# Kernel optimization log

Measured on AMD Instinct MI355X. Metric: run time of the kernel, lower is better.

The kernel has to match this reference:

```python
import jax, jax.numpy as jnp
import numpy as np

D = 128
N_COLS = 64
EPS = 1e-6
# op MLP index per feature token: mult, add, cos, absdiff, sub_ab, sub_ba, div_ab, div_ba
MLP_IDX = np.array([0, 1, 2, 3, 4, 4, 5, 5])


def setup_inputs() -> dict:
    key = jax.random.key(0)
    ks = jax.random.split(key, 16)
    B = 64
    pairs = np.array([(i, j) for i in range(N_COLS) for j in range(i + 1, N_COLS)], dtype=np.int32)
    P = pairs.shape[0]  # 2016
    s = 0.02
    inp = {
        "x": jax.random.normal(ks[0], (B, N_COLS, D), dtype=jnp.float32),
        "presence": jax.random.randint(ks[1], (B, N_COLS), 0, 2, dtype=jnp.int32),
        "idx_i": jnp.asarray(pairs[:, 0]),
        "idx_j": jnp.asarray(pairs[:, 1]),
        # 6 op MLPs (multiply, add, cosine, abs_diff, subtract, divide): d -> d/2 -> d
        "ops_W1": jax.random.normal(ks[2], (6, D, D // 2), dtype=jnp.float32) * s,
        "ops_b1": jnp.zeros((6, D // 2), dtype=jnp.float32),
        "ops_W2": jax.random.normal(ks[3], (6, D // 2, D), dtype=jnp.float32) * s,
        "ops_b2": jnp.zeros((6, D), dtype=jnp.float32),
        # presence MLP: 4 -> d/2 -> d
        "pres_W1": jax.random.normal(ks[4], (4, D // 2), dtype=jnp.float32) * s,
        "pres_b1": jnp.zeros((D // 2,), dtype=jnp.float32),
        "pres_W2": jax.random.normal(ks[5], (D // 2, D), dtype=jnp.float32) * s,
        "pres_b2": jnp.zeros((D,), dtype=jnp.float32),
        # fusion MLP: 9d -> 2d -> d
        "fus_W1": jax.random.normal(ks[6], (9 * D, 2 * D), dtype=jnp.float32) * s,
        "fus_b1": jnp.zeros((2 * D,), dtype=jnp.float32),
        "fus_W2": jax.random.normal(ks[7], (2 * D, D), dtype=jnp.float32) * s,
        "fus_b2": jnp.zeros((D,), dtype=jnp.float32),
    }
    return inp


def reference(x, presence, idx_i, idx_j,
              ops_W1, ops_b1, ops_W2, ops_b2,
              pres_W1, pres_b1, pres_W2, pres_b2,
              fus_W1, fus_b1, fus_W2, fus_b2):
    B = x.shape[0]
    P = idx_i.shape[0]
    A = x[:, idx_i]  # [B, P, D]
    Bv = x[:, idx_j]  # [B, P, D]
    An = A / (jnp.linalg.norm(A, axis=-1, keepdims=True) + EPS)
    Bn = Bv / (jnp.linalg.norm(Bv, axis=-1, keepdims=True) + EPS)
    # 8 elementwise relation features [8, B, P, D]
    feats = jnp.stack([
        A * Bv,                 # multiply
        A + Bv,                 # add
        An * Bn,                # cosine (elementwise normalized product)
        jnp.abs(A - Bv),        # abs diff
        A - Bv,                 # subtract A->B
        Bv - A,                 # subtract B->A
        A / (Bv + EPS),         # divide A/B
        Bv / (A + EPS),         # divide B/A
    ])
    W1 = ops_W1[MLP_IDX]  # [8, D, D/2]
    b1 = ops_b1[MLP_IDX]
    W2 = ops_W2[MLP_IDX]
    b2 = ops_b2[MLP_IDX]
    h = jax.nn.relu(jnp.einsum('kbpd,kdh->kbph', feats, W1) + b1[:, None, None, :])
    tok = jnp.einsum('kbph,khd->kbpd', h, W2) + b2[:, None, None, :]  # [8, B, P, D]
    # presence flags [B, P, 4]
    pa = presence[:, idx_i].astype(x.dtype)
    pb = presence[:, idx_j].astype(x.dtype)
    flags = jnp.stack([pa * pb, pa * (1 - pb), (1 - pa) * pb, (1 - pa) * (1 - pb)], axis=-1)
    ptok = jax.nn.relu(flags @ pres_W1 + pres_b1) @ pres_W2 + pres_b2  # [B, P, D]
    # concat 9 tokens -> fusion MLP -> 1 token per pair
    cat = jnp.concatenate([jnp.transpose(tok, (1, 2, 0, 3)).reshape(B, P, 8 * D), ptok], axis=-1)
    out = jax.nn.relu(cat @ fus_W1 + fus_b1) @ fus_W2 + fus_b2  # [B, P, D]
    return out
```

## Files before the change

### kernel.cpp

```cpp
#include <hip/hip_runtime.h>

#define EPS 1e-6f

using bfrag = __attribute__((ext_vector_type(8))) short;
using ffrag = __attribute__((ext_vector_type(4))) float;
typedef unsigned short ushortT;

#define MFMA(a, b, c) __builtin_amdgcn_mfma_f32_16x16x32_bf16((a), (b), (c), 0, 0, 0)

__device__ __forceinline__ ushortT bf_hi(float x) {
  unsigned u = __builtin_bit_cast(unsigned, x);
  return (ushortT)((u + 0x7FFFu + ((u >> 16) & 1u)) >> 16);
}
__device__ __forceinline__ float uaf(unsigned u) { return __builtin_bit_cast(float, u); }
__device__ __forceinline__ unsigned cvtpk(float a, float b) {
  unsigned d;
  asm("v_cvt_pk_bf16_f32 %0, %1, %2" : "=v"(d) : "v"(a), "v"(b));
  return d;
}
__device__ __forceinline__ int op_of(int k) { return (k < 4) ? k : ((k >> 1) + 2); }

__constant__ const int KMAP_host_dummy = 0;

__global__ void prologue(const float* __restrict__ ops_W1,
                         const float* __restrict__ ops_W2,
                         const float* __restrict__ ops_b2,
                         const float* __restrict__ pres_W1,
                         const float* __restrict__ pres_b1,
                         const float* __restrict__ pres_W2,
                         const float* __restrict__ pres_b2,
                         const float* __restrict__ fus_W1,
                         const float* __restrict__ fus_b1,
                         const float* __restrict__ fus_W2,
                         ushortT* __restrict__ Gp,
                         ushortT* __restrict__ W1p,
                         ushortT* __restrict__ W2p,
                         float* __restrict__ cb) {
  const int blk = blockIdx.x;
  const int tid = threadIdx.x;

  if (blk < 512) {
    int r = blk, n = tid;
    int slot = r >> 6;
    const int KMAP[8] = {0, 2, 3, 4, 1, 5, 6, 7};
    int k = KMAP[slot];
    int op = op_of(k);
    const float* w2 = ops_W2 + (size_t)(op * 64 + (r & 63)) * 128;
    const float* w1 = fus_W1 + (size_t)(k * 128) * 256 + n;
    float a0 = 0.f, a1 = 0.f, a2 = 0.f, a3 = 0.f;
#pragma unroll 8
    for (int d = 0; d < 128; d += 4) {
      a0 = fmaf(w2[d], w1[(size_t)d * 256], a0);
      a1 = fmaf(w2[d + 1], w1[(size_t)(d + 1) * 256], a1);
      a2 = fmaf(w2[d + 2], w1[(size_t)(d + 2) * 256], a2);
      a3 = fmaf(w2[d + 3], w1[(size_t)(d + 3) * 256], a3);
    }
    float acc = (a0 + a1) + (a2 + a3);
    int nt = n >> 4, kk = r >> 5, quad = (r >> 3) & 3, j = r & 7;
    int lane = quad * 16 + (n & 15);
    Gp[((nt * 16 + kk) * 64 + lane) * 8 + j] = bf_hi(acc);
  } else if (blk < 544) {
    int gid = (blk - 512) * 256 + tid;
    int lane = gid & 63, kk = (gid >> 6) & 3, nt = (gid >> 8) & 3, k = gid >> 10;
    int op = op_of(k);
    int col = nt * 16 + (lane & 15);
#pragma unroll
    for (int j = 0; j < 8; ++j) {
      int d = kk * 32 + ((lane >> 4) & 3) * 8 + j;
      W1p[gid * 8 + j] = bf_hi(ops_W1[((size_t)op * 128 + d) * 64 + col]);
    }
  } else if (blk < 560) {
    int gid = (blk - 544) * 256 + tid;
    int lane = gid & 63, kk = (gid >> 6) & 7, nt = gid >> 9;
    int col = nt * 16 + (lane & 15);
#pragma unroll
    for (int j = 0; j < 8; ++j) {
      int d = kk * 32 + ((lane >> 4) & 3) * 8 + j;
      W2p[gid * 8 + j] = bf_hi(fus_W2[(size_t)d * 128 + col]);
    }
  } else {
    int c = blk - 560, n = tid;
    __shared__ float hrelu[64];
    __shared__ float ptok[128];
    if (n < 64) hrelu[n] = fmaxf(pres_W1[c * 64 + n] + pres_b1[n], 0.f);
    __syncthreads();
    if (n < 128) {
      float p0 = pres_b2[n], p1 = 0.f;
#pragma unroll 8
      for (int hh = 0; hh < 64; hh += 2) {
        p0 = fmaf(hrelu[hh], pres_W2[hh * 128 + n], p0);
        p1 = fmaf(hrelu[hh + 1], pres_W2[(hh + 1) * 128 + n], p1);
      }
      ptok[n] = p0 + p1;
    }
    __syncthreads();
    float acc = fus_b1[n];
#pragma unroll 4
    for (int d = 0; d < 128; ++d)
      acc = fmaf(ptok[d], fus_W1[(size_t)(1024 + d) * 256 + n], acc);
    float acc2 = 0.f;
    for (int k = 0; k < 8; ++k) {
      int op = op_of(k);
#pragma unroll 4
      for (int d = 0; d < 128; ++d)
        acc2 = fmaf(ops_b2[op * 128 + d], fus_W1[(size_t)(k * 128 + d) * 256 + n], acc2);
    }
    cb[c * 256 + n] = acc + acc2;
  }
}

__device__ __forceinline__ void ldX(const float* Xrow, int quad, float (&r)[32]) {
#pragma unroll
  for (int kk = 0; kk < 4; ++kk) {
    float4 t0 = *(const float4*)(Xrow + kk * 32 + quad * 8);
    float4 t1 = *(const float4*)(Xrow + kk * 32 + quad * 8 + 4);
    r[kk * 8 + 0] = t0.x; r[kk * 8 + 1] = t0.y; r[kk * 8 + 2] = t0.z; r[kk * 8 + 3] = t0.w;
    r[kk * 8 + 4] = t1.x; r[kk * 8 + 5] = t1.y; r[kk * 8 + 6] = t1.z; r[kk * 8 + 7] = t1.w;
  }
}

struct Frag2 {
  bfrag h[4];
  bfrag l[4];
};

union U4 {
  unsigned u[4];
  bfrag b;
};

#define FM_MUL 0
#define FM_ADD 1
#define FM_SUB 2
#define FM_DAB 3
#define FM_DBA 4

template <int M>
__device__ __forceinline__ void buildFrags(const float (&af)[32], const float (&bf)[32],
                                           Frag2& fr) {
#pragma unroll
  for (int kk = 0; kk < 4; ++kk) {
    U4 uh, ul;
#pragma unroll
    for (int p = 0; p < 4; ++p) {
      float a0 = af[kk * 8 + 2 * p],     b0 = bf[kk * 8 + 2 * p];
      float a1 = af[kk * 8 + 2 * p + 1], b1 = bf[kk * 8 + 2 * p + 1];
      float f0, f1;
      if constexpr (M == FM_MUL)      { f0 = a0 * b0; f1 = a1 * b1; }
      else if constexpr (M == FM_ADD) { f0 = a0 + b0; f1 = a1 + b1; }
      else if constexpr (M == FM_SUB) { f0 = a0 - b0; f1 = a1 - b1; }
      else if constexpr (M == FM_DAB) {
        f0 = a0 * __builtin_amdgcn_rcpf(b0 + EPS);
        f1 = a1 * __builtin_amdgcn_rcpf(b1 + EPS);
      } else {
        f0 = b0 * __builtin_amdgcn_rcpf(a0 + EPS);
        f1 = b1 * __builtin_amdgcn_rcpf(a1 + EPS);
      }
      unsigned dh = cvtpk(f0, f1);
      float r0 = f0 - uaf(dh << 16);
      float r1 = f1 - uaf(dh & 0xFFFF0000u);
      uh.u[p] = dh;
      ul.u[p] = cvtpk(r0, r1);
    }
    fr.h[kk] = uh.b;
    fr.l[kk] = ul.b;
  }
}

template <int K>
__device__ __forceinline__ ffrag mmW1(const Frag2& fr, int wv, int lane,
                                      const ushortT* __restrict__ W1p) {
  const ushortT* wp = W1p + ((K * 4 + wv) * 4) * 512 + lane * 8;
  ffrag s = {0.f, 0.f, 0.f, 0.f};
#pragma unroll
  for (int kk = 0; kk < 4; ++kk) {
    bfrag w = *(const bfrag*)(wp + kk * 512);
    s = MFMA(fr.h[kk], w, s);
    s = MFMA(fr.l[kk], w, s);
  }
  return s;
}

template <int K>
__device__ __forceinline__ ffrag mmW1Abs(const Frag2& fr, int wv, int lane,
                                         const ushortT* __restrict__ W1p) {
  const ushortT* wp = W1p + ((K * 4 + wv) * 4) * 512 + lane * 8;
  ffrag s = {0.f, 0.f, 0.f, 0.f};
#pragma unroll
  for (int kk = 0; kk < 4; ++kk) {
    U4 h, l, ha, la;
    h.b = fr.h[kk];
    l.b = fr.l[kk];
#pragma unroll
    for (int p = 0; p < 4; ++p) {
      ha.u[p] = h.u[p] & 0x7FFF7FFFu;
      la.u[p] = l.u[p] ^ (h.u[p] & 0x80008000u);
    }
    bfrag w = *(const bfrag*)(wp + kk * 512);
    s = MFMA(ha.b, w, s);
    s = MFMA(la.b, w, s);
  }
  return s;
}

__device__ __forceinline__ void storeH(ffrag s, float scl, float bias, int rbase, int col,
                                       ushortT (*Hh)[136], ushortT (*Hl)[136]) {
  float v[4];
#pragma unroll
  for (int i = 0; i < 4; ++i) v[i] = fmaxf(fmaf(s[i], scl, bias), 0.f);
#pragma unroll
  for (int p = 0; p < 2; ++p) {
    unsigned dh = cvtpk(v[2 * p], v[2 * p + 1]);
    float r0 = v[2 * p] - uaf(dh << 16);
    float r1 = v[2 * p + 1] - uaf(dh & 0xFFFF0000u);
    unsigned dl = cvtpk(r0, r1);
    Hh[rbase + 2 * p][col] = (ushortT)(dh & 0xFFFFu);
    Hh[rbase + 2 * p + 1][col] = (ushortT)(dh >> 16);
    Hl[rbase + 2 * p][col] = (ushortT)(dl & 0xFFFFu);
    Hl[rbase + 2 * p + 1][col] = (ushortT)(dl >> 16);
  }
}

__device__ __forceinline__ void p3round(int r, int wv, int lane, int quad, int c0,
                                        ushortT (*Hh)[136], ushortT (*Hl)[136],
                                        const ushortT* __restrict__ Gp,
                                        ffrag (&u)[4], ffrag (&v)[4]) {
#pragma unroll
  for (int kk = 0; kk < 4; ++kk) {
    bfrag ah0 = *(const bfrag*)&Hh[c0][kk * 32 + quad * 8];
    bfrag al0 = *(const bfrag*)&Hl[c0][kk * 32 + quad * 8];
    bfrag ah1 = *(const bfrag*)&Hh[16 + c0][kk * 32 + quad * 8];
    bfrag al1 = *(const bfrag*)&Hl[16 + c0][kk * 32 + quad * 8];
#pragma unroll
    for (int nt4 = 0; nt4 < 4; ++nt4) {
      bfrag g = *(const bfrag*)(Gp + (((wv * 4 + nt4) * 16 + r * 4 + kk) * 64 + lane) * 8);
      u[nt4] = MFMA(ah0, g, u[nt4]);
      u[nt4] = MFMA(al0, g, u[nt4]);
      v[nt4] = MFMA(ah1, g, v[nt4]);
      v[nt4] = MFMA(al1, g, v[nt4]);
    }
  }
}

__global__ __launch_bounds__(256, 3)
void drel_main(const float* __restrict__ x, const int* __restrict__ presence,
               const int* __restrict__ idx_i, const int* __restrict__ idx_j,
               const float* __restrict__ ops_b1, const float* __restrict__ fus_b2,
               const ushortT* __restrict__ W1p, const ushortT* __restrict__ Gp,
               const ushortT* __restrict__ W2p, const float* __restrict__ cbias,
               float* __restrict__ out) {
  __shared__ __align__(16) char smem[51328];
  float   (*Xs)[132]  = reinterpret_cast<float(*)[132]>(smem);
  ushortT (*Hh)[136]  = reinterpret_cast<ushortT(*)[136]>(smem + 33792);
  ushortT (*Hl)[136]  = reinterpret_cast<ushortT(*)[136]>(smem + 42496);
  ushortT (*Dh)[264]  = reinterpret_cast<ushortT(*)[264]>(smem + 33792);
  int* sCombo = reinterpret_cast<int*>(smem + 51200);

  const int tid = threadIdx.x;
  const int wv = tid >> 6, lane = tid & 63, quad = lane >> 4, c0 = lane & 15;

  const int blk = blockIdx.x;
  const int b = blk / 63;
  const int p0 = (blk % 63) * 32;

  const float* xb = x + (size_t)b * 64 * 128;
#pragma unroll
  for (int it = 0; it < 8; ++it) {
    int i = tid + it * 256;
    int row = i >> 5, c4 = (i & 31) * 4;
    *(float4*)&Xs[row][c4] = *(const float4*)(xb + row * 128 + c4);
  }
  if (tid < 32) {
    int p = p0 + tid;
    int pa = presence[b * 64 + idx_i[p]];
    int pb = presence[b * 64 + idx_j[p]];
    sCombo[tid] = pa ? (pb ? 0 : 1) : (pb ? 2 : 3);
  }

  const int ri0 = idx_i[p0 + c0],      rj0 = idx_j[p0 + c0];
  const int ri1 = idx_i[p0 + 16 + c0], rj1 = idx_j[p0 + 16 + c0];

  const int bcol = wv * 16 + c0;
  const float bb0 = ops_b1[0 * 64 + bcol];
  const float bb1_ = ops_b1[1 * 64 + bcol];
  const float bb2 = ops_b1[2 * 64 + bcol];
  const float bb3 = ops_b1[3 * 64 + bcol];
  const float bb4 = ops_b1[4 * 64 + bcol];
  const float bb5 = ops_b1[5 * 64 + bcol];

  ffrag u[4], v[4];
  __syncthreads();
  {
    int comb0[4], comb1[4];
#pragma unroll
    for (int i = 0; i < 4; ++i) {
      comb0[i] = sCombo[quad * 4 + i];
      comb1[i] = sCombo[16 + quad * 4 + i];
    }
#pragma unroll
    for (int nt4 = 0; nt4 < 4; ++nt4) {
      int col = (wv * 4 + nt4) * 16 + c0;
#pragma unroll
      for (int i = 0; i < 4; ++i) {
        u[nt4][i] = cbias[comb0[i] * 256 + col];
        v[nt4][i] = cbias[comb1[i] * 256 + col];
      }
    }
  }

  float af[32], bf[32];
  ffrag s4t0, s4t1;

  {
    ldX(Xs[ri0], quad, af); ldX(Xs[rj0], quad, bf);
    float sa = 0.f, sb = 0.f;
#pragma unroll
    for (int q = 0; q < 32; ++q) { sa = fmaf(af[q], af[q], sa); sb = fmaf(bf[q], bf[q], sb); }
    sa += __shfl_xor(sa, 16); sb += __shfl_xor(sb, 16);
    sa += __shfl_xor(sa, 32); sb += __shfl_xor(sb, 32);
    float scl = (1.f / (sqrtf(sa) + EPS)) * (1.f / (sqrtf(sb) + EPS));
    Frag2 fr;
    buildFrags<FM_MUL>(af, bf, fr);
    ffrag s0 = mmW1<0>(fr, wv, lane, W1p);
    ffrag s2 = mmW1<2>(fr, wv, lane, W1p);
    storeH(s0, 1.f, bb0, 0 * 16 + quad * 4, bcol, Hh, Hl);
    storeH(s2, scl, bb2, 0 * 16 + quad * 4, 64 + bcol, Hh, Hl);

    ldX(Xs[ri1], quad, af); ldX(Xs[rj1], quad, bf);
    sa = 0.f; sb = 0.f;
#pragma unroll
    for (int q = 0; q < 32; ++q) { sa = fmaf(af[q], af[q], sa); sb = fmaf(bf[q], bf[q], sb); }
    sa += __shfl_xor(sa, 16); sb += __shfl_xor(sb, 16);
    sa += __shfl_xor(sa, 32); sb += __shfl_xor(sb, 32);
    scl = (1.f / (sqrtf(sa) + EPS)) * (1.f / (sqrtf(sb) + EPS));
    buildFrags<FM_MUL>(af, bf, fr);
    s0 = mmW1<0>(fr, wv, lane, W1p);
    s2 = mmW1<2>(fr, wv, lane, W1p);
    storeH(s0, 1.f, bb0, 1 * 16 + quad * 4, bcol, Hh, Hl);
    storeH(s2, scl, bb2, 1 * 16 + quad * 4, 64 + bcol, Hh, Hl);
  }
  __syncthreads();
  p3round(0, wv, lane, quad, c0, Hh, Hl, Gp, u, v);
  __syncthreads();

  {
    ldX(Xs[ri0], quad, af); ldX(Xs[rj0], quad, bf);
    Frag2 fr;
    buildFrags<FM_SUB>(af, bf, fr);
    s4t0 = mmW1<4>(fr, wv, lane, W1p);
    ffrag s3 = mmW1Abs<3>(fr, wv, lane, W1p);
    storeH(s3, 1.f, bb3, 0 * 16 + quad * 4, bcol, Hh, Hl);
    storeH(s4t0, 1.f, bb4, 0 * 16 + quad * 4, 64 + bcol, Hh, Hl);

    ldX(Xs[ri1], quad, af); ldX(Xs[rj1], quad, bf);
    buildFrags<FM_SUB>(af, bf, fr);
    s4t1 = mmW1<4>(fr, wv, lane, W1p);
    s3 = mmW1Abs<3>(fr, wv, lane, W1p);
    storeH(s3, 1.f, bb3, 1 * 16 + quad * 4, bcol, Hh, Hl);
    storeH(s4t1, 1.f, bb4, 1 * 16 + quad * 4, 64 + bcol, Hh, Hl);
  }
  __syncthreads();
  p3round(1, wv, lane, quad, c0, Hh, Hl, Gp, u, v);
  __syncthreads();

  {
    ldX(Xs[ri0], quad, af); ldX(Xs[rj0], quad, bf);
    Frag2 fr;
    buildFrags<FM_ADD>(af, bf, fr);
    ffrag s1 = mmW1<1>(fr, wv, lane, W1p);
    storeH(s1, 1.f, bb1_, 0 * 16 + quad * 4, bcol, Hh, Hl);
    storeH(s4t0, -1.f, bb4, 0 * 16 + quad * 4, 64 + bcol, Hh, Hl);

    ldX(Xs[ri1], quad, af); ldX(Xs[rj1], quad, bf);
    buildFrags<FM_ADD>(af, bf, fr);
    s1 = mmW1<1>(fr, wv, lane, W1p);
    storeH(s1, 1.f, bb1_, 1 * 16 + quad * 4, bcol, Hh, Hl);
    storeH(s4t1, -1.f, bb4, 1 * 16 + quad * 4, 64 + bcol, Hh, Hl);
  }
  __syncthreads();
  p3round(2, wv, lane, quad, c0, Hh, Hl, Gp, u, v);
  __syncthreads();

  {
    ldX(Xs[ri0], quad, af); ldX(Xs[rj0], quad, bf);
    Frag2 fr;
    buildFrags<FM_DAB>(af, bf, fr);
    ffrag s6 = mmW1<6>(fr, wv, lane, W1p);
    buildFrags<FM_DBA>(af, bf, fr);
    ffrag s7 = mmW1<7>(fr, wv, lane, W1p);
    storeH(s6, 1.f, bb5, 0 * 16 + quad * 4, bcol, Hh, Hl);
    storeH(s7, 1.f, bb5, 0 * 16 + quad * 4, 64 + bcol, Hh, Hl);

    ldX(Xs[ri1], quad, af); ldX(Xs[rj1], quad, bf);
    buildFrags<FM_DAB>(af, bf, fr);
    s6 = mmW1<6>(fr, wv, lane, W1p);
    buildFrags<FM_DBA>(af, bf, fr);
    s7 = mmW1<7>(fr, wv, lane, W1p);
    storeH(s6, 1.f, bb5, 1 * 16 + quad * 4, bcol, Hh, Hl);
    storeH(s7, 1.f, bb5, 1 * 16 + quad * 4, 64 + bcol, Hh, Hl);
  }
  __syncthreads();
  p3round(3, wv, lane, quad, c0, Hh, Hl, Gp, u, v);
  __syncthreads();

#pragma unroll
  for (int nt4 = 0; nt4 < 4; ++nt4) {
    int col = (wv * 4 + nt4) * 16 + c0;
#pragma unroll
    for (int p = 0; p < 2; ++p) {
      unsigned du = cvtpk(fmaxf(u[nt4][2 * p], 0.f), fmaxf(u[nt4][2 * p + 1], 0.f));
      Dh[quad * 4 + 2 * p][col] = (ushortT)(du & 0xFFFFu);
      Dh[quad * 4 + 2 * p + 1][col] = (ushortT)(du >> 16);
      unsigned dv = cvtpk(fmaxf(v[nt4][2 * p], 0.f), fmaxf(v[nt4][2 * p + 1], 0.f));
      Dh[16 + quad * 4 + 2 * p][col] = (ushortT)(dv & 0xFFFFu);
      Dh[16 + quad * 4 + 2 * p + 1][col] = (ushortT)(dv >> 16);
    }
  }
  __syncthreads();

  ffrag o[2], q[2];
#pragma unroll
  for (int nt2 = 0; nt2 < 2; ++nt2) {
    float bias = fus_b2[(wv * 2 + nt2) * 16 + c0];
    o[nt2] = ffrag{bias, bias, bias, bias};
    q[nt2] = o[nt2];
  }
#pragma unroll
  for (int kk = 0; kk < 8; ++kk) {
    bfrag dh0 = *(const bfrag*)&Dh[c0][kk * 32 + quad * 8];
    bfrag dh1 = *(const bfrag*)&Dh[16 + c0][kk * 32 + quad * 8];
#pragma unroll
    for (int nt2 = 0; nt2 < 2; ++nt2) {
      bfrag w = *(const bfrag*)(W2p + (((wv * 2 + nt2) * 8 + kk) * 64 + lane) * 8);
      o[nt2] = MFMA(dh0, w, o[nt2]);
      q[nt2] = MFMA(dh1, w, q[nt2]);
    }
  }
#pragma unroll
  for (int nt2 = 0; nt2 < 2; ++nt2) {
    int col = (wv * 2 + nt2) * 16 + c0;
#pragma unroll
    for (int i = 0; i < 4; ++i) {
      int row = quad * 4 + i;
      out[(size_t)(b * 2016 + p0 + row) * 128 + col] = o[nt2][i];
      out[(size_t)(b * 2016 + p0 + 16 + row) * 128 + col] = q[nt2][i];
    }
  }
}

extern "C" void kernel_launch(void* const* d_in, const int* in_sizes, int n_in,
                              void* d_out, int out_size, void* d_ws, size_t ws_size,
                              hipStream_t stream) {
  const float* x        = (const float*)d_in[0];
  const int*   presence = (const int*)d_in[1];
  const int*   idx_i    = (const int*)d_in[2];
  const int*   idx_j    = (const int*)d_in[3];
  const float* ops_W1   = (const float*)d_in[4];
  const float* ops_b1   = (const float*)d_in[5];
  const float* ops_W2   = (const float*)d_in[6];
  const float* ops_b2   = (const float*)d_in[7];
  const float* pres_W1  = (const float*)d_in[8];
  const float* pres_b1  = (const float*)d_in[9];
  const float* pres_W2  = (const float*)d_in[10];
  const float* pres_b2  = (const float*)d_in[11];
  const float* fus_W1   = (const float*)d_in[12];
  const float* fus_b1   = (const float*)d_in[13];
  const float* fus_W2   = (const float*)d_in[14];
  const float* fus_b2   = (const float*)d_in[15];

  char* ws = (char*)d_ws;
  ushortT* Gp  = (ushortT*)(ws);
  ushortT* W1p = (ushortT*)(ws + 262144);
  ushortT* W2p = (ushortT*)(ws + 393216);
  float*   CB  = (float*)(ws + 458752);

  prologue<<<564, 256, 0, stream>>>(ops_W1, ops_W2, ops_b2, pres_W1, pres_b1,
                                    pres_W2, pres_b2, fus_W1, fus_b1, fus_W2,
                                    Gp, W1p, W2p, CB);
  drel_main<<<4032, 256, 0, stream>>>(x, presence, idx_i, idx_j, ops_b1, fus_b2,
                                      W1p, Gp, W2p, CB, (float*)d_out);
}
```

Baseline: 281.7 us.

## Split first-layer op MLP work across waves by pair tile and op role

Each wave now owns one 16-pair tile and one op (role) and computes all four 16-column output tiles of that op's hidden layer, instead of every wave doing both pair tiles and both ops for one column slice. This removes redundant feature building, norm computation and frag conversion, since each wave builds fragments only for its own op and tile. The abs-diff op now builds its own fragments with fabsf instead of bit-masking subtract fragments. The cost is that each wave loads all W1 column tiles for its op, and waves with different roles may do unequal work, notably in round 2 where the subtract-reuse role only stores.

After: 259.8 us. 7.8% less time.

```diff
diff --git a/kernel.cpp b/kernel.cpp
--- a/kernel.cpp
+++ b/kernel.cpp
@@ -19,8 +19,6 @@
   return d;
 }
 __device__ __forceinline__ int op_of(int k) { return (k < 4) ? k : ((k >> 1) + 2); }
-
-__constant__ const int KMAP_host_dummy = 0;
 
 __global__ void prologue(const float* __restrict__ ops_W1,
                          const float* __restrict__ ops_W2,
@@ -132,8 +130,9 @@
 #define FM_MUL 0
 #define FM_ADD 1
 #define FM_SUB 2
-#define FM_DAB 3
-#define FM_DBA 4
+#define FM_ABS 3
+#define FM_DAB 4
+#define FM_DBA 5
 
 template <int M>
 __device__ __forceinline__ void buildFrags(const float (&af)[32], const float (&bf)[32],
@@ -149,6 +148,7 @@
       if constexpr (M == FM_MUL)      { f0 = a0 * b0; f1 = a1 * b1; }
       else if constexpr (M == FM_ADD) { f0 = a0 + b0; f1 = a1 + b1; }
       else if constexpr (M == FM_SUB) { f0 = a0 - b0; f1 = a1 - b1; }
+      else if constexpr (M == FM_ABS) { f0 = fabsf(a0 - b0); f1 = fabsf(a1 - b1); }
       else if constexpr (M == FM_DAB) {
         f0 = a0 * __builtin_amdgcn_rcpf(b0 + EPS);
         f1 = a1 * __builtin_amdgcn_rcpf(b1 + EPS);
@@ -168,39 +168,26 @@
 }
 
 template <int K>
-__device__ __forceinline__ ffrag mmW1(const Frag2& fr, int wv, int lane,
-                                      const ushortT* __restrict__ W1p) {
-  const ushortT* wp = W1p + ((K * 4 + wv) * 4) * 512 + lane * 8;
-  ffrag s = {0.f, 0.f, 0.f, 0.f};
-#pragma unroll
-  for (int kk = 0; kk < 4; ++kk) {
-    bfrag w = *(const bfrag*)(wp + kk * 512);
-    s = MFMA(fr.h[kk], w, s);
-    s = MFMA(fr.l[kk], w, s);
-  }
-  return s;
-}
-
-template <int K>
-__device__ __forceinline__ ffrag mmW1Abs(const Frag2& fr, int wv, int lane,
-                                         const ushortT* __restrict__ W1p) {
-  const ushortT* wp = W1p + ((K * 4 + wv) * 4) * 512 + lane * 8;
-  ffrag s = {0.f, 0.f, 0.f, 0.f};
-#pragma unroll
-  for (int kk = 0; kk < 4; ++kk) {
-    U4 h, l, ha, la;
-    h.b = fr.h[kk];
-    l.b = fr.l[kk];
-#pragma unroll
-    for (int p = 0; p < 4; ++p) {
-      ha.u[p] = h.u[p] & 0x7FFF7FFFu;
-      la.u[p] = l.u[p] ^ (h.u[p] & 0x80008000u);
-    }
-    bfrag w = *(const bfrag*)(wp + kk * 512);
-    s = MFMA(ha.b, w, s);
-    s = MFMA(la.b, w, s);
-  }
-  return s;
+__device__ __forceinline__ void mmAll(const Frag2& fr, int lane,
+                                      const ushortT* __restrict__ W1p, ffrag (&s)[4]) {
+#pragma unroll
+  for (int nt = 0; nt < 4; ++nt) {
+    const ushortT* wp = W1p + ((K * 4 + nt) * 4) * 512 + lane * 8;
+    ffrag acc = {0.f, 0.f, 0.f, 0.f};
+#pragma unroll
+    for (int kk = 0; kk < 4; ++kk) {
+      bfrag w = *(const bfrag*)(wp + kk * 512);
+      acc = MFMA(fr.h[kk], w, acc);
+      acc = MFMA(fr.l[kk], w, acc);
+    }
+    s[nt] = acc;
+  }
+}
+
+__device__ __forceinline__ void ldBias(const float* __restrict__ ops_b1, int OP, int c0,
+                                       float (&bb)[4]) {
+#pragma unroll
+  for (int nt = 0; nt < 4; ++nt) bb[nt] = ops_b1[OP * 64 + nt * 16 + c0];
 }
 
 __device__ __forceinline__ void storeH(ffrag s, float scl, float bias, int rbase, int col,
@@ -219,6 +206,14 @@
     Hl[rbase + 2 * p][col] = (ushortT)(dl & 0xFFFFu);
     Hl[rbase + 2 * p + 1][col] = (ushortT)(dl >> 16);
   }
+}
+
+__device__ __forceinline__ void storeH4(const ffrag (&s)[4], float scl, const float (&bb)[4],
+                                        int rbase, int colbase, int c0,
+                                        ushortT (*Hh)[136], ushortT (*Hl)[136]) {
+#pragma unroll
+  for (int nt = 0; nt < 4; ++nt)
+    storeH(s[nt], scl, bb[nt], rbase, colbase + nt * 16 + c0, Hh, Hl);
 }
 
 __device__ __forceinline__ void p3round(int r, int wv, int lane, int quad, int c0,
@@ -258,6 +253,8 @@
 
   const int tid = threadIdx.x;
   const int wv = tid >> 6, lane = tid & 63, quad = lane >> 4, c0 = lane & 15;
+  const int wtile = wv & 1;
+  const int wrole = wv >> 1;
 
   const int blk = blockIdx.x;
   const int b = blk / 63;
@@ -277,16 +274,9 @@
     sCombo[tid] = pa ? (pb ? 0 : 1) : (pb ? 2 : 3);
   }
 
-  const int ri0 = idx_i[p0 + c0],      rj0 = idx_j[p0 + c0];
-  const int ri1 = idx_i[p0 + 16 + c0], rj1 = idx_j[p0 + 16 + c0];
-
-  const int bcol = wv * 16 + c0;
-  const float bb0 = ops_b1[0 * 64 + bcol];
-  const float bb1_ = ops_b1[1 * 64 + bcol];
-  const float bb2 = ops_b1[2 * 64 + bcol];
-  const float bb3 = ops_b1[3 * 64 + bcol];
-  const float bb4 = ops_b1[4 * 64 + bcol];
-  const float bb5 = ops_b1[5 * 64 + bcol];
+  const int rI = idx_i[p0 + wtile * 16 + c0];
+  const int rJ = idx_j[p0 + wtile * 16 + c0];
+  const int rbase = wtile * 16 + quad * 4;
 
   ffrag u[4], v[4];
   __syncthreads();
@@ -309,95 +299,86 @@
   }
 
   float af[32], bf[32];
-  ffrag s4t0, s4t1;
+  Frag2 fr;
+  ffrag s4[4];
 
   {
-    ldX(Xs[ri0], quad, af); ldX(Xs[rj0], quad, bf);
-    float sa = 0.f, sb = 0.f;
-#pragma unroll
-    for (int q = 0; q < 32; ++q) { sa = fmaf(af[q], af[q], sa); sb = fmaf(bf[q], bf[q], sb); }
-    sa += __shfl_xor(sa, 16); sb += __shfl_xor(sb, 16);
-    sa += __shfl_xor(sa, 32); sb += __shfl_xor(sb, 32);
-    float scl = (1.f / (sqrtf(sa) + EPS)) * (1.f / (sqrtf(sb) + EPS));
-    Frag2 fr;
+    ldX(Xs[rI], quad, af); ldX(Xs[rJ], quad, bf);
     buildFrags<FM_MUL>(af, bf, fr);
-    ffrag s0 = mmW1<0>(fr, wv, lane, W1p);
-    ffrag s2 = mmW1<2>(fr, wv, lane, W1p);
-    storeH(s0, 1.f, bb0, 0 * 16 + quad * 4, bcol, Hh, Hl);
-    storeH(s2, scl, bb2, 0 * 16 + quad * 4, 64 + bcol, Hh, Hl);
-
-    ldX(Xs[ri1], quad, af); ldX(Xs[rj1], quad, bf);
-    sa = 0.f; sb = 0.f;
-#pragma unroll
-    for (int q = 0; q < 32; ++q) { sa = fmaf(af[q], af[q], sa); sb = fmaf(bf[q], bf[q], sb); }
-    sa += __shfl_xor(sa, 16); sb += __shfl_xor(sb, 16);
-    sa += __shfl_xor(sa, 32); sb += __shfl_xor(sb, 32);
-    scl = (1.f / (sqrtf(sa) + EPS)) * (1.f / (sqrtf(sb) + EPS));
-    buildFrags<FM_MUL>(af, bf, fr);
-    s0 = mmW1<0>(fr, wv, lane, W1p);
-    s2 = mmW1<2>(fr, wv, lane, W1p);
-    storeH(s0, 1.f, bb0, 1 * 16 + quad * 4, bcol, Hh, Hl);
-    storeH(s2, scl, bb2, 1 * 16 + quad * 4, 64 + bcol, Hh, Hl);
+    ffrag s[4];
+    float bb[4];
+    if (wrole == 0) {
+      ldBias(ops_b1, 0, c0, bb);
+      mmAll<0>(fr, lane, W1p, s);
+      storeH4(s, 1.f, bb, rbase, 0, c0, Hh, Hl);
+    } else {
+      float sa = 0.f, sb = 0.f;
+#pragma unroll
+      for (int q = 0; q < 32; ++q) { sa = fmaf(af[q], af[q], sa); sb = fmaf(bf[q], bf[q], sb); }
+      sa += __shfl_xor(sa, 16); sb += __shfl_xor(sb, 16);
+      sa += __shfl_xor(sa, 32); sb += __shfl_xor(sb, 32);
+      float scl = (1.f / (sqrtf(sa) + EPS)) * (1.f / (sqrtf(sb) + EPS));
+      ldBias(ops_b1, 2, c0, bb);
+      mmAll<2>(fr, lane, W1p, s);
+      storeH4(s, scl, bb, rbase, 64, c0, Hh, Hl);
+    }
   }
   __syncthreads();
   p3round(0, wv, lane, quad, c0, Hh, Hl, Gp, u, v);
   __syncthreads();
 
   {
-    ldX(Xs[ri0], quad, af); ldX(Xs[rj0], quad, bf);
-    Frag2 fr;
-    buildFrags<FM_SUB>(af, bf, fr);
-    s4t0 = mmW1<4>(fr, wv, lane, W1p);
-    ffrag s3 = mmW1Abs<3>(fr, wv, lane, W1p);
-    storeH(s3, 1.f, bb3, 0 * 16 + quad * 4, bcol, Hh, Hl);
-    storeH(s4t0, 1.f, bb4, 0 * 16 + quad * 4, 64 + bcol, Hh, Hl);
-
-    ldX(Xs[ri1], quad, af); ldX(Xs[rj1], quad, bf);
-    buildFrags<FM_SUB>(af, bf, fr);
-    s4t1 = mmW1<4>(fr, wv, lane, W1p);
-    s3 = mmW1Abs<3>(fr, wv, lane, W1p);
-    storeH(s3, 1.f, bb3, 1 * 16 + quad * 4, bcol, Hh, Hl);
-    storeH(s4t1, 1.f, bb4, 1 * 16 + quad * 4, 64 + bcol, Hh, Hl);
+    ldX(Xs[rI], quad, af); ldX(Xs[rJ], quad, bf);
+    float bb[4];
+    if (wrole == 0) {
+      buildFrags<FM_ABS>(af, bf, fr);
+      ffrag s[4];
+      ldBias(ops_b1, 3, c0, bb);
+      mmAll<3>(fr, lane, W1p, s);
+      storeH4(s, 1.f, bb, rbase, 0, c0, Hh, Hl);
+    } else {
+      buildFrags<FM_SUB>(af, bf, fr);
+      ldBias(ops_b1, 4, c0, bb);
+      mmAll<4>(fr, lane, W1p, s4);
+      storeH4(s4, 1.f, bb, rbase, 64, c0, Hh, Hl);
+    }
   }
   __syncthreads();
   p3round(1, wv, lane, quad, c0, Hh, Hl, Gp, u, v);
   __syncthreads();
 
   {
-    ldX(Xs[ri0], quad, af); ldX(Xs[rj0], quad, bf);
-    Frag2 fr;
-    buildFrags<FM_ADD>(af, bf, fr);
-    ffrag s1 = mmW1<1>(fr, wv, lane, W1p);
-    storeH(s1, 1.f, bb1_, 0 * 16 + quad * 4, bcol, Hh, Hl);
-    storeH(s4t0, -1.f, bb4, 0 * 16 + quad * 4, 64 + bcol, Hh, Hl);
-
-    ldX(Xs[ri1], quad, af); ldX(Xs[rj1], quad, bf);
-    buildFrags<FM_ADD>(af, bf, fr);
-    s1 = mmW1<1>(fr, wv, lane, W1p);
-    storeH(s1, 1.f, bb1_, 1 * 16 + quad * 4, bcol, Hh, Hl);
-    storeH(s4t1, -1.f, bb4, 1 * 16 + quad * 4, 64 + bcol, Hh, Hl);
+    float bb[4];
+    if (wrole == 0) {
+      ldX(Xs[rI], quad, af); ldX(Xs[rJ], quad, bf);
+      buildFrags<FM_ADD>(af, bf, fr);
+      ffrag s[4];
+      ldBias(ops_b1, 1, c0, bb);
+      mmAll<1>(fr, lane, W1p, s);
+      storeH4(s, 1.f, bb, rbase, 0, c0, Hh, Hl);
+    } else {
+      ldBias(ops_b1, 4, c0, bb);
+      storeH4(s4, -1.f, bb, rbase, 64, c0, Hh, Hl);
+    }
   }
   __syncthreads();
   p3round(2, wv, lane, quad, c0, Hh, Hl, Gp, u, v);
   __syncthreads();
 
   {
-    ldX(Xs[ri0], quad, af); ldX(Xs[rj0], quad, bf);
-    Frag2 fr;
-    buildFrags<FM_DAB>(af, bf, fr);
-    ffrag s6 = mmW1<6>(fr, wv, lane, W1p);
-    buildFrags<FM_DBA>(af, bf, fr);
-    ffrag s7 = mmW1<7>(fr, wv, lane, W1p);
-    storeH(s6, 1.f, bb5, 0 * 16 + quad * 4, bcol, Hh, Hl);
-    storeH(s7, 1.f, bb5, 0 * 16 + quad * 4, 64 + bcol, Hh, Hl);
-
-    ldX(Xs[ri1], quad, af); ldX(Xs[rj1], quad, bf);
-    buildFrags<FM_DAB>(af, bf, fr);
-    s6 = mmW1<6>(fr, wv, lane, W1p);
-    buildFrags<FM_DBA>(af, bf, fr);
-    s7 = mmW1<7>(fr, wv, lane, W1p);
-    storeH(s6, 1.f, bb5, 1 * 16 + quad * 4, bcol, Hh, Hl);
-    storeH(s7, 1.f, bb5, 1 * 16 + quad * 4, 64 + bcol, Hh, Hl);
+    ldX(Xs[rI], quad, af); ldX(Xs[rJ], quad, bf);
+    ffrag s[4];
+    float bb[4];
+    ldBias(ops_b1, 5, c0, bb);
+    if (wrole == 0) {
+      buildFrags<FM_DAB>(af, bf, fr);
+      mmAll<6>(fr, lane, W1p, s);
+      storeH4(s, 1.f, bb, rbase, 0, c0, Hh, Hl);
+    } else {
+      buildFrags<FM_DBA>(af, bf, fr);
+      mmAll<7>(fr, lane, W1p, s);
+      storeH4(s, 1.f, bb, rbase, 64, c0, Hh, Hl);
+    }
   }
   __syncthreads();
   p3round(3, wv, lane, quad, c0, Hh, Hl, Gp, u, v);
```
